# Kernel optimization log

Measured on AMD Instinct MI355X. Metric: run time of the kernel, lower is better.

## Reference

```python
import jax, jax.numpy as jnp
import numpy as np

# Fixed Db4 filters (non-learnable buffers in the original module)
_H = np.array([-0.010597401785069032, 0.032883011666982945, 0.030841381835560764,
               -0.18703481171888114, -0.02798376941698385, 0.6308807679295904,
               0.7148465705529155, 0.2303778133088964], dtype=np.float32)
_G = np.array([(-1.0) ** k * v for k, v in enumerate(_H[::-1])], dtype=np.float32)

LEVELS = 5  # max(1, floor(log2(256)) - 3)


def _dwt_level(x, filt):
    """reflect-pad left (K-1), depthwise cross-correlation, stride-2 decimation.
    Equivalent to torch: F.pad(x,(K-1,0),'reflect') -> conv1d(groups=C) -> [..., ::2].
    Fused into a single strided conv since out[::2] == stride-2 conv from offset 0."""
    K = filt.shape[0]
    C = x.shape[1]
    xp = jnp.pad(x, ((0, 0), (0, 0), (K - 1, 0)), mode='reflect')
    w = jnp.broadcast_to(filt.reshape(1, 1, K), (C, 1, K))  # (C,1,K) depthwise
    return jax.lax.conv_general_dilated(
        xp, w, window_strides=(2,), padding='VALID',
        dimension_numbers=('NCH', 'OIH', 'NCH'), feature_group_count=C)


def _forward(x, db4_low, db4_high):
    approx = x
    details = []
    for _ in range(LEVELS):
        low = _dwt_level(approx, db4_low)
        high = _dwt_level(approx, db4_high)
        details.append(high)
        approx = low
    Fd = approx                    # final approximation  (B,C,S/32)
    Ft = details[-1]               # (B,C,S/32)
    Fa = details[-2]               # (B,C,S/16)
    Fb = details[-3]               # (B,C,S/8)
    Fg = details[-4]               # (B,C,S/4)
    FR = jnp.concatenate([Fd, Ft, Fa, Fb, Fg], axis=2)
    return (Fd, Ft, Fa, Fb, Fg, FR)


def setup_inputs() -> dict:
    key = jax.random.key(0)
    x = jax.random.normal(key, (64, 64, 16384), dtype=jnp.float32)
    return {"x": x, "db4_low": jnp.asarray(_H), "db4_high": jnp.asarray(_G)}


def reference(x, db4_low, db4_high):
    return _forward(x, db4_low, db4_high)
```

## Files before the change

### kernel.cpp

```cpp
#include <hip/hip_runtime.h>


static constexpr int SLEN = 16384;

typedef float f32x4 __attribute__((ext_vector_type(4)));

__device__ __forceinline__ int swz4(int f) {
    const int s = f >> 2;
    return (s ^ ((s >> 3) & 7)) << 2;
}
__device__ __forceinline__ int swz1(int f) {
    const int s = f >> 2;
    return (((s ^ ((s >> 3) & 7)) << 2) | (f & 3));
}

__device__ __forceinline__ float dotH(const float* w) {
    float s =      -0.010597401785069032f * w[0];
    s = fmaf( 0.032883011666982945f, w[1], s);
    s = fmaf( 0.030841381835560764f, w[2], s);
    s = fmaf(-0.18703481171888114f,  w[3], s);
    s = fmaf(-0.02798376941698385f,  w[4], s);
    s = fmaf( 0.6308807679295904f,   w[5], s);
    s = fmaf( 0.7148465705529155f,   w[6], s);
    s = fmaf( 0.2303778133088964f,   w[7], s);
    return s;
}
__device__ __forceinline__ float dotG(const float* w) {
    float s =       0.2303778133088964f * w[0];
    s = fmaf(-0.7148465705529155f,   w[1], s);
    s = fmaf( 0.6308807679295904f,   w[2], s);
    s = fmaf( 0.02798376941698385f,  w[3], s);
    s = fmaf(-0.18703481171888114f,  w[4], s);
    s = fmaf(-0.030841381835560764f, w[5], s);
    s = fmaf( 0.032883011666982945f, w[6], s);
    s = fmaf( 0.010597401785069032f, w[7], s);
    return s;
}

__device__ __forceinline__ void loadw16g(const float* __restrict__ src, int q, float* w) {
    if (q == 0) {
#pragma unroll
        for (int i = 0; i < 16; ++i) { int m = i - 8; m = (m < 0) ? -m : m; w[i] = src[m]; }
    } else {
        const float4 v0 = *(const float4*)(src + 8 * q - 8);
        const float4 v1 = *(const float4*)(src + 8 * q - 4);
        const float4 v2 = *(const float4*)(src + 8 * q);
        const float4 v3 = *(const float4*)(src + 8 * q + 4);
        w[0]  = v0.x; w[1]  = v0.y; w[2]  = v0.z; w[3]  = v0.w;
        w[4]  = v1.x; w[5]  = v1.y; w[6]  = v1.z; w[7]  = v1.w;
        w[8]  = v2.x; w[9]  = v2.y; w[10] = v2.z; w[11] = v2.w;
        w[12] = v3.x; w[13] = v3.y; w[14] = v3.z; w[15] = v3.w;
    }
}

__device__ __forceinline__ void lw16s(const float* __restrict__ base, int foff, float* w) {
#pragma unroll
    for (int j = 0; j < 4; ++j) {
        const float4 v = *(const float4*)(base + swz4(foff + 4 * j));
        w[4*j+0] = v.x; w[4*j+1] = v.y; w[4*j+2] = v.z; w[4*j+3] = v.w;
    }
}
__device__ __forceinline__ void lw16s_q0(const float* __restrict__ base, float* w) {
#pragma unroll
    for (int i = 0; i < 16; ++i) { int m = i - 8; m = (m < 0) ? -m : m; w[i] = base[swz1(m)]; }
}

__device__ __forceinline__ void ntst4(float* p, float a0, float a1, float a2, float a3) {
    f32x4 v; v.x = a0; v.y = a1; v.z = a2; v.w = a3;
    __builtin_nontemporal_store(v, (f32x4*)p);
}

__device__ __forceinline__ void barrier_lds() {
    asm volatile("s_waitcnt lgkmcnt(0)" ::: "memory");
    __builtin_amdgcn_s_barrier();
    asm volatile("" ::: "memory");
}

__global__ __launch_bounds__(256, 8)
void dwt5_kernel(const float* __restrict__ x, float* __restrict__ out)
{
    __shared__ float buf[3264];
    const int bid = blockIdx.x;
    const int r   = bid >> 2;
    const int h   = bid & 3;
    const int tid = threadIdx.x;

    const float* __restrict__ xr = x + (size_t)r * SLEN;
    const size_t frBase = (size_t)33554432 + (size_t)r * 8192;

    const int A1s = h ? 2048*h - 120 : 0;
    const int A2s = h ? 1024*h - 56  : 0;
    const int A3s = h ?  512*h - 24  : 0;
    const int A4s = h ?  256*h - 8   : 0;
    constexpr int REG2 = 2176;
    constexpr int REG4 = 1024;

    {
        const int g1lo = A1s >> 2;
        const int g1hi = 512 * (h + 1);
#pragma unroll
        for (int jj = 0; jj < 3; ++jj) {
            const int g = g1lo + tid + jj * 256;
            if (g < g1hi) {
                float w[16];
                loadw16g(xr, g, w);
                const float a0 = dotH(w + 1), a1 = dotH(w + 3), a2 = dotH(w + 5), a3 = dotH(w + 7);
                *(float4*)(buf + swz4(4 * g - A1s)) = make_float4(a0, a1, a2, a3);
            }
        }
    }
    barrier_lds();

    {
        const int g2lo = A2s >> 2;
        const int g2hi = 256 * (h + 1);
        const int gd   = 256 * h;
        float* __restrict__ hi1 = out + (size_t)16777216 + (size_t)r * 4096;
        float* __restrict__ hi2 = out + frBase + 4096;
#pragma unroll
        for (int jj = 0; jj < 2; ++jj) {
            const int g = g2lo + tid + jj * 256;
            if (g < g2hi) {
                float w[16];
                if (g == 0) lw16s_q0(buf, w);
                else        lw16s(buf, 8 * g - 8 - A1s, w);
                const float a0 = dotH(w + 1), a1 = dotH(w + 3), a2 = dotH(w + 5), a3 = dotH(w + 7);
                *(float4*)(buf + REG2 + swz4(4 * g - A2s)) = make_float4(a0, a1, a2, a3);
                if (g >= gd) {
                    const float d0 = dotG(w + 1), d1 = dotG(w + 3), d2 = dotG(w + 5), d3 = dotG(w + 7);
                    ntst4(hi1 + 4 * g, d0, d1, d2, d3);
                    ntst4(hi2 + 4 * g, d0, d1, d2, d3);
                }
            }
        }
    }
    barrier_lds();

    {
        const int g3lo = A3s >> 2;
        const int g3hi = 128 * (h + 1);
        const int gd   = 128 * h;
        float* __restrict__ hi1 = out + (size_t)8388608 + (size_t)r * 2048;
        float* __restrict__ hi2 = out + frBase + 2048;
        const int g = g3lo + tid;
        if (g < g3hi) {
            float w[16];
            if (g == 0) lw16s_q0(buf + REG2, w);
            else        lw16s(buf + REG2, 8 * g - 8 - A2s, w);
            const float a0 = dotH(w + 1), a1 = dotH(w + 3), a2 = dotH(w + 5), a3 = dotH(w + 7);
            *(float4*)(buf + swz4(4 * g - A3s)) = make_float4(a0, a1, a2, a3);
            if (g >= gd) {
                const float d0 = dotG(w + 1), d1 = dotG(w + 3), d2 = dotG(w + 5), d3 = dotG(w + 7);
                ntst4(hi1 + 4 * g, d0, d1, d2, d3);
                ntst4(hi2 + 4 * g, d0, d1, d2, d3);
            }
        }
    }
    barrier_lds();

    {
        const int g4lo = A4s >> 2;
        const int g4hi = 64 * (h + 1);
        const int gd   = 64 * h;
        float* __restrict__ hi1 = out + (size_t)4194304 + (size_t)r * 1024;
        float* __restrict__ hi2 = out + frBase + 1024;
        const int g = g4lo + tid;
        if (g < g4hi) {
            float w[16];
            if (g == 0) lw16s_q0(buf, w);
            else        lw16s(buf, 8 * g - 8 - A3s, w);
            const float a0 = dotH(w + 1), a1 = dotH(w + 3), a2 = dotH(w + 5), a3 = dotH(w + 7);
            *(float4*)(buf + REG4 + swz4(4 * g - A4s)) = make_float4(a0, a1, a2, a3);
            if (g >= gd) {
                const float d0 = dotG(w + 1), d1 = dotG(w + 3), d2 = dotG(w + 5), d3 = dotG(w + 7);
                ntst4(hi1 + 4 * g, d0, d1, d2, d3);
                ntst4(hi2 + 4 * g, d0, d1, d2, d3);
            }
        }
    }
    barrier_lds();

    if (tid < 32) {
        const int g = 32 * h + tid;
        float w[16];
        if (g == 0) lw16s_q0(buf + REG4, w);
        else        lw16s(buf + REG4, 8 * g - 8 - A4s, w);
        const float a0 = dotH(w + 1), a1 = dotH(w + 3), a2 = dotH(w + 5), a3 = dotH(w + 7);
        const float d0 = dotG(w + 1), d1 = dotG(w + 3), d2 = dotG(w + 5), d3 = dotG(w + 7);
        ntst4(out + (size_t)r * 512 + 4 * g,                   a0, a1, a2, a3);
        ntst4(out + frBase + 4 * g,                            a0, a1, a2, a3);
        ntst4(out + (size_t)2097152 + (size_t)r * 512 + 4 * g, d0, d1, d2, d3);
        ntst4(out + frBase + 512 + 4 * g,                      d0, d1, d2, d3);
    }
}

extern "C" void kernel_launch(void* const* d_in, const int* in_sizes, int n_in,
                              void* d_out, int out_size, void* d_ws, size_t ws_size,
                              hipStream_t stream) {
    const float* x = (const float*)d_in[0];
    float* out = (float*)d_out;
    dwt5_kernel<<<16384, 256, 0, stream>>>(x, out);
}
```

Baseline: 86.57 us.

## Stage input rows into LDS via direct global-to-LDS loads before level one

Level one no longer reads its overlapping 16-float windows straight from global memory. The block first copies its input slice into LDS with global_load_lds (16-byte, swizzled addressing) and then reads windows from LDS using the existing swizzle helpers. The LDS buffer doubles in size and the region layout changes to hold the raw input alongside the intermediate levels. Occupancy is lowered to 6 blocks per CU in exchange, and all loads must complete before a barrier, so there is no overlap between loading and compute.

Result: faster. 84.04 us, median of 2 (-2.9%).

```diff
diff --git a/kernel.cpp b/kernel.cpp
--- a/kernel.cpp
+++ b/kernel.cpp
@@ -37,22 +37,6 @@
     return s;
 }
 
-__device__ __forceinline__ void loadw16g(const float* __restrict__ src, int q, float* w) {
-    if (q == 0) {
-#pragma unroll
-        for (int i = 0; i < 16; ++i) { int m = i - 8; m = (m < 0) ? -m : m; w[i] = src[m]; }
-    } else {
-        const float4 v0 = *(const float4*)(src + 8 * q - 8);
-        const float4 v1 = *(const float4*)(src + 8 * q - 4);
-        const float4 v2 = *(const float4*)(src + 8 * q);
-        const float4 v3 = *(const float4*)(src + 8 * q + 4);
-        w[0]  = v0.x; w[1]  = v0.y; w[2]  = v0.z; w[3]  = v0.w;
-        w[4]  = v1.x; w[5]  = v1.y; w[6]  = v1.z; w[7]  = v1.w;
-        w[8]  = v2.x; w[9]  = v2.y; w[10] = v2.z; w[11] = v2.w;
-        w[12] = v3.x; w[13] = v3.y; w[14] = v3.z; w[15] = v3.w;
-    }
-}
-
 __device__ __forceinline__ void lw16s(const float* __restrict__ base, int foff, float* w) {
 #pragma unroll
     for (int j = 0; j < 4; ++j) {
@@ -68,6 +52,12 @@
 __device__ __forceinline__ void ntst4(float* p, float a0, float a1, float a2, float a3) {
     f32x4 v; v.x = a0; v.y = a1; v.z = a2; v.w = a3;
     __builtin_nontemporal_store(v, (f32x4*)p);
+}
+
+__device__ __forceinline__ void gl_lds16(const float* gp, float* lp) {
+    __builtin_amdgcn_global_load_lds(
+        (const __attribute__((address_space(1))) void*)gp,
+        (__attribute__((address_space(3))) void*)lp, 16, 0, 0);
 }
 
 __device__ __forceinline__ void barrier_lds() {
@@ -76,10 +66,10 @@
     asm volatile("" ::: "memory");
 }
 
-__global__ __launch_bounds__(256, 8)
+__global__ __launch_bounds__(256, 6)
 void dwt5_kernel(const float* __restrict__ x, float* __restrict__ out)
 {
-    __shared__ float buf[3264];
+    __shared__ float buf[6528];
     const int bid = blockIdx.x;
     const int r   = bid >> 2;
     const int h   = bid & 3;
@@ -88,12 +78,32 @@
     const float* __restrict__ xr = x + (size_t)r * SLEN;
     const size_t frBase = (size_t)33554432 + (size_t)r * 8192;
 
+    const int X0  = h ? 4096*h - 256 : 0;
     const int A1s = h ? 2048*h - 120 : 0;
     const int A2s = h ? 1024*h - 56  : 0;
     const int A3s = h ?  512*h - 24  : 0;
     const int A4s = h ?  256*h - 8   : 0;
-    constexpr int REG2 = 2176;
-    constexpr int REG4 = 1024;
+    constexpr int RA1 = 4352;
+    constexpr int RA2 = 0;
+    constexpr int RA3 = 2048;
+    constexpr int RA4 = 3072;
+
+    {
+        const float* xsrc = xr + X0;
+#pragma unroll
+        for (int j = 0; j < 4; ++j) {
+            const int L  = tid + 256*j;
+            const int Ls = L ^ ((L >> 3) & 7);
+            gl_lds16(xsrc + 4*Ls, buf + 4*L);
+        }
+        if (h != 0 && tid < 64) {
+            const int L  = tid + 1024;
+            const int Ls = L ^ ((L >> 3) & 7);
+            gl_lds16(xsrc + 4*Ls, buf + 4*L);
+        }
+        asm volatile("s_waitcnt vmcnt(0)" ::: "memory");
+    }
+    barrier_lds();
 
     {
         const int g1lo = A1s >> 2;
@@ -103,9 +113,10 @@
             const int g = g1lo + tid + jj * 256;
             if (g < g1hi) {
                 float w[16];
-                loadw16g(xr, g, w);
+                if (g == 0) lw16s_q0(buf, w);
+                else        lw16s(buf, 8 * g - 8 - X0, w);
                 const float a0 = dotH(w + 1), a1 = dotH(w + 3), a2 = dotH(w + 5), a3 = dotH(w + 7);
-                *(float4*)(buf + swz4(4 * g - A1s)) = make_float4(a0, a1, a2, a3);
+                *(float4*)(buf + RA1 + swz4(4 * g - A1s)) = make_float4(a0, a1, a2, a3);
             }
         }
     }
@@ -122,10 +133,10 @@
             const int g = g2lo + tid + jj * 256;
             if (g < g2hi) {
                 float w[16];
-                if (g == 0) lw16s_q0(buf, w);
-                else        lw16s(buf, 8 * g - 8 - A1s, w);
+                if (g == 0) lw16s_q0(buf + RA1, w);
+                else        lw16s(buf + RA1, 8 * g - 8 - A1s, w);
                 const float a0 = dotH(w + 1), a1 = dotH(w + 3), a2 = dotH(w + 5), a3 = dotH(w + 7);
-                *(float4*)(buf + REG2 + swz4(4 * g - A2s)) = make_float4(a0, a1, a2, a3);
+                *(float4*)(buf + RA2 + swz4(4 * g - A2s)) = make_float4(a0, a1, a2, a3);
                 if (g >= gd) {
                     const float d0 = dotG(w + 1), d1 = dotG(w + 3), d2 = dotG(w + 5), d3 = dotG(w + 7);
                     ntst4(hi1 + 4 * g, d0, d1, d2, d3);
@@ -145,10 +156,10 @@
         const int g = g3lo + tid;
         if (g < g3hi) {
             float w[16];
-            if (g == 0) lw16s_q0(buf + REG2, w);
-            else        lw16s(buf + REG2, 8 * g - 8 - A2s, w);
+            if (g == 0) lw16s_q0(buf + RA2, w);
+            else        lw16s(buf + RA2, 8 * g - 8 - A2s, w);
             const float a0 = dotH(w + 1), a1 = dotH(w + 3), a2 = dotH(w + 5), a3 = dotH(w + 7);
-            *(float4*)(buf + swz4(4 * g - A3s)) = make_float4(a0, a1, a2, a3);
+            *(float4*)(buf + RA3 + swz4(4 * g - A3s)) = make_float4(a0, a1, a2, a3);
             if (g >= gd) {
                 const float d0 = dotG(w + 1), d1 = dotG(w + 3), d2 = dotG(w + 5), d3 = dotG(w + 7);
                 ntst4(hi1 + 4 * g, d0, d1, d2, d3);
@@ -167,10 +178,10 @@
         const int g = g4lo + tid;
         if (g < g4hi) {
             float w[16];
-            if (g == 0) lw16s_q0(buf, w);
-            else        lw16s(buf, 8 * g - 8 - A3s, w);
+            if (g == 0) lw16s_q0(buf + RA3, w);
+            else        lw16s(buf + RA3, 8 * g - 8 - A3s, w);
             const float a0 = dotH(w + 1), a1 = dotH(w + 3), a2 = dotH(w + 5), a3 = dotH(w + 7);
-            *(float4*)(buf + REG4 + swz4(4 * g - A4s)) = make_float4(a0, a1, a2, a3);
+            *(float4*)(buf + RA4 + swz4(4 * g - A4s)) = make_float4(a0, a1, a2, a3);
             if (g >= gd) {
                 const float d0 = dotG(w + 1), d1 = dotG(w + 3), d2 = dotG(w + 5), d3 = dotG(w + 7);
                 ntst4(hi1 + 4 * g, d0, d1, d2, d3);
@@ -183,8 +194,8 @@
     if (tid < 32) {
         const int g = 32 * h + tid;
         float w[16];
-        if (g == 0) lw16s_q0(buf + REG4, w);
-        else        lw16s(buf + REG4, 8 * g - 8 - A4s, w);
+        if (g == 0) lw16s_q0(buf + RA4, w);
+        else        lw16s(buf + RA4, 8 * g - 8 - A4s, w);
         const float a0 = dotH(w + 1), a1 = dotH(w + 3), a2 = dotH(w + 5), a3 = dotH(w + 7);
         const float d0 = dotG(w + 1), d1 = dotG(w + 3), d2 = dotG(w + 5), d3 = dotG(w + 7);
         ntst4(out + (size_t)r * 512 + 4 * g,                   a0, a1, a2, a3);
```

## Process two rows per block to amortize barriers and halve grid size

Applied to the files above, without the earlier changes.

Each block now handles two signal rows, with a doubled shared buffer and per-stage loops over both rows, so every barrier is shared by twice the work and the grid shrinks to half as many blocks. This targets barrier and launch overhead and the idle threads in the later, narrow stages. In exchange, per-block LDS doubles and the launch-bounds occupancy hint drops from 8 to 6, which may reduce resident waves and latency hiding for this memory-bound kernel.

Result: slower. 91.01 us (+5.1%).

```diff
diff --git a/kernel.cpp b/kernel.cpp
--- a/kernel.cpp
+++ b/kernel.cpp
@@ -76,17 +76,14 @@
     asm volatile("" ::: "memory");
 }
 
-__global__ __launch_bounds__(256, 8)
+__global__ __launch_bounds__(256, 6)
 void dwt5_kernel(const float* __restrict__ x, float* __restrict__ out)
 {
-    __shared__ float buf[3264];
+    __shared__ float buf[6528];
     const int bid = blockIdx.x;
-    const int r   = bid >> 2;
+    const int rp  = bid >> 2;
     const int h   = bid & 3;
     const int tid = threadIdx.x;
-
-    const float* __restrict__ xr = x + (size_t)r * SLEN;
-    const size_t frBase = (size_t)33554432 + (size_t)r * 8192;
 
     const int A1s = h ? 2048*h - 120 : 0;
     const int A2s = h ? 1024*h - 56  : 0;
@@ -94,8 +91,13 @@
     const int A4s = h ?  256*h - 8   : 0;
     constexpr int REG2 = 2176;
     constexpr int REG4 = 1024;
-
-    {
+    constexpr int ROWB = 3264;
+
+#pragma unroll
+    for (int rr = 0; rr < 2; ++rr) {
+        const int r = 2*rp + rr;
+        const float* __restrict__ xr = x + (size_t)r * SLEN;
+        float* const bb = buf + rr * ROWB;
         const int g1lo = A1s >> 2;
         const int g1hi = 512 * (h + 1);
 #pragma unroll
@@ -105,13 +107,17 @@
                 float w[16];
                 loadw16g(xr, g, w);
                 const float a0 = dotH(w + 1), a1 = dotH(w + 3), a2 = dotH(w + 5), a3 = dotH(w + 7);
-                *(float4*)(buf + swz4(4 * g - A1s)) = make_float4(a0, a1, a2, a3);
-            }
-        }
-    }
-    barrier_lds();
-
-    {
+                *(float4*)(bb + swz4(4 * g - A1s)) = make_float4(a0, a1, a2, a3);
+            }
+        }
+    }
+    barrier_lds();
+
+#pragma unroll
+    for (int rr = 0; rr < 2; ++rr) {
+        const int r = 2*rp + rr;
+        const size_t frBase = (size_t)33554432 + (size_t)r * 8192;
+        float* const bb = buf + rr * ROWB;
         const int g2lo = A2s >> 2;
         const int g2hi = 256 * (h + 1);
         const int gd   = 256 * h;
@@ -122,10 +128,10 @@
             const int g = g2lo + tid + jj * 256;
             if (g < g2hi) {
                 float w[16];
-                if (g == 0) lw16s_q0(buf, w);
-                else        lw16s(buf, 8 * g - 8 - A1s, w);
+                if (g == 0) lw16s_q0(bb, w);
+                else        lw16s(bb, 8 * g - 8 - A1s, w);
                 const float a0 = dotH(w + 1), a1 = dotH(w + 3), a2 = dotH(w + 5), a3 = dotH(w + 7);
-                *(float4*)(buf + REG2 + swz4(4 * g - A2s)) = make_float4(a0, a1, a2, a3);
+                *(float4*)(bb + REG2 + swz4(4 * g - A2s)) = make_float4(a0, a1, a2, a3);
                 if (g >= gd) {
                     const float d0 = dotG(w + 1), d1 = dotG(w + 3), d2 = dotG(w + 5), d3 = dotG(w + 7);
                     ntst4(hi1 + 4 * g, d0, d1, d2, d3);
@@ -136,7 +142,11 @@
     }
     barrier_lds();
 
-    {
+#pragma unroll
+    for (int rr = 0; rr < 2; ++rr) {
+        const int r = 2*rp + rr;
+        const size_t frBase = (size_t)33554432 + (size_t)r * 8192;
+        float* const bb = buf + rr * ROWB;
         const int g3lo = A3s >> 2;
         const int g3hi = 128 * (h + 1);
         const int gd   = 128 * h;
@@ -145,10 +155,10 @@
         const int g = g3lo + tid;
         if (g < g3hi) {
             float w[16];
-            if (g == 0) lw16s_q0(buf + REG2, w);
-            else        lw16s(buf + REG2, 8 * g - 8 - A2s, w);
+            if (g == 0) lw16s_q0(bb + REG2, w);
+            else        lw16s(bb + REG2, 8 * g - 8 - A2s, w);
             const float a0 = dotH(w + 1), a1 = dotH(w + 3), a2 = dotH(w + 5), a3 = dotH(w + 7);
-            *(float4*)(buf + swz4(4 * g - A3s)) = make_float4(a0, a1, a2, a3);
+            *(float4*)(bb + swz4(4 * g - A3s)) = make_float4(a0, a1, a2, a3);
             if (g >= gd) {
                 const float d0 = dotG(w + 1), d1 = dotG(w + 3), d2 = dotG(w + 5), d3 = dotG(w + 7);
                 ntst4(hi1 + 4 * g, d0, d1, d2, d3);
@@ -158,7 +168,11 @@
     }
     barrier_lds();
 
-    {
+#pragma unroll
+    for (int rr = 0; rr < 2; ++rr) {
+        const int r = 2*rp + rr;
+        const size_t frBase = (size_t)33554432 + (size_t)r * 8192;
+        float* const bb = buf + rr * ROWB;
         const int g4lo = A4s >> 2;
         const int g4hi = 64 * (h + 1);
         const int gd   = 64 * h;
@@ -167,10 +181,10 @@
         const int g = g4lo + tid;
         if (g < g4hi) {
             float w[16];
-            if (g == 0) lw16s_q0(buf, w);
-            else        lw16s(buf, 8 * g - 8 - A3s, w);
+            if (g == 0) lw16s_q0(bb, w);
+            else        lw16s(bb, 8 * g - 8 - A3s, w);
             const float a0 = dotH(w + 1), a1 = dotH(w + 3), a2 = dotH(w + 5), a3 = dotH(w + 7);
-            *(float4*)(buf + REG4 + swz4(4 * g - A4s)) = make_float4(a0, a1, a2, a3);
+            *(float4*)(bb + REG4 + swz4(4 * g - A4s)) = make_float4(a0, a1, a2, a3);
             if (g >= gd) {
                 const float d0 = dotG(w + 1), d1 = dotG(w + 3), d2 = dotG(w + 5), d3 = dotG(w + 7);
                 ntst4(hi1 + 4 * g, d0, d1, d2, d3);
@@ -180,11 +194,16 @@
     }
     barrier_lds();
 
-    if (tid < 32) {
-        const int g = 32 * h + tid;
+    if (tid < 64) {
+        const int rr = tid >> 5;
+        const int t  = tid & 31;
+        const int r = 2*rp + rr;
+        const size_t frBase = (size_t)33554432 + (size_t)r * 8192;
+        float* const bb = buf + rr * ROWB;
+        const int g = 32 * h + t;
         float w[16];
-        if (g == 0) lw16s_q0(buf + REG4, w);
-        else        lw16s(buf + REG4, 8 * g - 8 - A4s, w);
+        if (g == 0) lw16s_q0(bb + REG4, w);
+        else        lw16s(bb + REG4, 8 * g - 8 - A4s, w);
         const float a0 = dotH(w + 1), a1 = dotH(w + 3), a2 = dotH(w + 5), a3 = dotH(w + 7);
         const float d0 = dotG(w + 1), d1 = dotG(w + 3), d2 = dotG(w + 5), d3 = dotG(w + 7);
         ntst4(out + (size_t)r * 512 + 4 * g,                   a0, a1, a2, a3);
@@ -199,5 +218,5 @@
                               hipStream_t stream) {
     const float* x = (const float*)d_in[0];
     float* out = (float*)d_out;
-    dwt5_kernel<<<16384, 256, 0, stream>>>(x, out);
-}
+    dwt5_kernel<<<8192, 256, 0, stream>>>(x, out);
+}
```
